# Kernel tuning notes

Measured on AMD Instinct MI355X. Metric: run time of the kernel, lower is better.

The kernel has to match this reference:

```python
import jax, jax.numpy as jnp
import numpy as np

N_NODES = 100000
N_EDGES = 1600000
IN_FEATS = 128
N_HIDDEN = 128
N_CLASSES = 40
EPS = 1e-12  # torch F.normalize eps


def _sage_conv(h, src, dst, W_self, b_self, W_neigh, b_neigh, act, norm):
    # mean aggregation over in-neighbors: dst receives from src
    agg = jax.ops.segment_sum(h[src], dst, num_segments=N_NODES)  # [N, D]
    deg = jax.ops.segment_sum(jnp.ones(dst.shape, h.dtype), dst, num_segments=N_NODES)
    h_neigh = agg / jnp.maximum(deg, 1.0)[:, None]
    out = h @ W_self + b_self + h_neigh @ W_neigh + b_neigh
    if act:
        out = jax.nn.relu(out)
    if norm:
        out = out / jnp.maximum(
            jnp.linalg.norm(out, axis=1, keepdims=True), EPS)
    return out


def setup_inputs() -> dict:
    key = jax.random.key(0)
    ks = jax.random.split(key, 16)
    def lin(k, fan_in, fan_out):
        s = 1.0 / np.sqrt(fan_in)
        return jax.random.uniform(k, (fan_in, fan_out), jnp.float32, -s, s)
    inp = {
        "features": jax.random.normal(ks[0], (N_NODES, IN_FEATS), jnp.float32),
        "src": jax.random.randint(ks[1], (N_EDGES,), 0, N_NODES, jnp.int32),
        "dst": jax.random.randint(ks[2], (N_EDGES,), 0, N_NODES, jnp.int32),
        # layer 0: in -> hidden
        "Ws0": lin(ks[3], IN_FEATS, N_HIDDEN), "bs0": jnp.zeros((N_HIDDEN,), jnp.float32),
        "Wn0": lin(ks[4], IN_FEATS, N_HIDDEN), "bn0": jnp.zeros((N_HIDDEN,), jnp.float32),
        # layer 1: hidden -> hidden
        "Ws1": lin(ks[5], N_HIDDEN, N_HIDDEN), "bs1": jnp.zeros((N_HIDDEN,), jnp.float32),
        "Wn1": lin(ks[6], N_HIDDEN, N_HIDDEN), "bn1": jnp.zeros((N_HIDDEN,), jnp.float32),
        # layer 2: hidden -> classes (no activation, no norm)
        "Ws2": lin(ks[7], N_HIDDEN, N_CLASSES), "bs2": jnp.zeros((N_CLASSES,), jnp.float32),
        "Wn2": lin(ks[8], N_HIDDEN, N_CLASSES), "bn2": jnp.zeros((N_CLASSES,), jnp.float32),
    }
    return inp


def reference(features, src, dst,
              Ws0, bs0, Wn0, bn0,
              Ws1, bs1, Wn1, bn1,
              Ws2, bs2, Wn2, bn2):
    h = _sage_conv(features, src, dst, Ws0, bs0, Wn0, bn0, act=True, norm=True)
    h = _sage_conv(h, src, dst, Ws1, bs1, Wn1, bn1, act=True, norm=True)
    out = _sage_conv(h, src, dst, Ws2, bs2, Wn2, bn2, act=False, norm=False)
    return out
```

## Files before the change

### kernel.cpp

```cpp
#include <hip/hip_runtime.h>
#include <hip/hip_bf16.h>

#define N_NODES_C 100000
#define N_EDGES_C 1600000
#define N_BUCK ((N_NODES_C + 255) / 256)
#define BCAP 4608
#define PART_NB 160
#define PART_CHUNK ((N_EDGES_C + PART_NB - 1) / PART_NB)

typedef __attribute__((ext_vector_type(8))) short          short8;
typedef __attribute__((ext_vector_type(4))) float          f32x4;
typedef __attribute__((ext_vector_type(4))) unsigned int   u32x4;
typedef __attribute__((ext_vector_type(4))) unsigned short u16x4;

__device__ inline float load1v(const void* p, size_t i, int bf) {
    return bf ? __bfloat162float(((const __hip_bfloat16*)p)[i])
              : ((const float*)p)[i];
}
__device__ inline unsigned short f2bf(float f) {
    __hip_bfloat16 h = __float2bfloat16(f);
    return *reinterpret_cast<unsigned short*>(&h);
}
__device__ inline float bf_lo(unsigned u) { return __uint_as_float(u << 16); }
__device__ inline float bf_hi(unsigned u) { return __uint_as_float(u & 0xffff0000u); }
__device__ inline void acc8(float* a, u32x4 r) {
    a[0] += bf_lo(r.x); a[1] += bf_hi(r.x);
    a[2] += bf_lo(r.y); a[3] += bf_hi(r.y);
    a[4] += bf_lo(r.z); a[5] += bf_hi(r.z);
    a[6] += bf_lo(r.w); a[7] += bf_hi(r.w);
}

__global__ void detect_init(const void* __restrict__ feats, int* __restrict__ gflag,
                            int* __restrict__ bcur) {
    const unsigned short* u = (const unsigned short*)feats;
    int bad = 0;
    for (int i = threadIdx.x; i < 2048; i += 64) {
        unsigned e = (u[i] >> 7) & 0xFF;
        if (e >= 0xC0) bad++;
    }
#pragma unroll
    for (int off = 32; off > 0; off >>= 1) bad += __shfl_down(bad, off, 64);
    if (threadIdx.x == 0) *gflag = (bad == 0) ? 1 : 0;
    for (int b = threadIdx.x; b < N_BUCK; b += 64) bcur[b] = b * BCAP;
}

__global__ __launch_bounds__(256) void partition2(
        const int* __restrict__ src, const int* __restrict__ dst,
        int* __restrict__ bcur, unsigned* __restrict__ pairs) {
    __shared__ int cnt[N_BUCK];
    __shared__ int lbase[N_BUCK];
    int tid = threadIdx.x;
    int e0 = blockIdx.x * PART_CHUNK;
    int e1 = min(e0 + PART_CHUNK, N_EDGES_C);
    for (int i = tid; i < N_BUCK; i += 256) cnt[i] = 0;
    __syncthreads();
    for (int e = e0 + tid; e < e1; e += 256)
        atomicAdd(&cnt[dst[e] >> 8], 1);
    __syncthreads();
    for (int i = tid; i < N_BUCK; i += 256) {
        int c = cnt[i];
        lbase[i] = c ? atomicAdd(&bcur[i], c) : 0;
        cnt[i] = 0;
    }
    __syncthreads();
    for (int e = e0 + tid; e < e1; e += 256) {
        int s = src[e], d = dst[e];
        int bk = d >> 8;
        int pos = lbase[bk] + atomicAdd(&cnt[bk], 1);
        pairs[pos] = ((unsigned)(d & 255) << 17) | (unsigned)s;
    }
}

__global__ void mkboff_kernel(const int* __restrict__ bcur, int* __restrict__ boff) {
    __shared__ int c[N_BUCK];
    int tid = threadIdx.x;
    for (int i = tid; i < N_BUCK; i += 64) c[i] = bcur[i] - i * BCAP;
    __syncthreads();
    if (tid == 0) {
        int run = 0;
        for (int b = 0; b < N_BUCK; ++b) { int t = c[b]; c[b] = run; run += t; }
        boff[N_BUCK] = run;
    }
    __syncthreads();
    for (int i = tid; i < N_BUCK; i += 64) boff[i] = c[i];
}

__global__ __launch_bounds__(256) void bucket_fill(
        const unsigned* __restrict__ pairs, const int* __restrict__ boff,
        int* __restrict__ csr, int* __restrict__ row_start, int* __restrict__ deg) {
    __shared__ int cnt[256], sd[256], lcur[256];
    int b = blockIdx.x, tid = threadIdx.x;
    int pbase = b * BCAP;
    int base = boff[b], count = boff[b + 1] - base;
    cnt[tid] = 0;
    __syncthreads();
    for (int i = tid; i < count; i += 256)
        atomicAdd(&cnt[pairs[pbase + i] >> 17], 1);
    __syncthreads();
    sd[tid] = cnt[tid];
    __syncthreads();
    for (int st = 1; st < 256; st <<= 1) {
        int t = (tid >= st) ? sd[tid - st] : 0;
        __syncthreads();
        sd[tid] += t;
        __syncthreads();
    }
    int excl = sd[tid] - cnt[tid];
    int node = b * 256 + tid;
    if (node < N_NODES_C) { row_start[node] = base + excl; deg[node] = cnt[tid]; }
    lcur[tid] = excl;
    __syncthreads();
    for (int i = tid; i < count; i += 256) {
        unsigned p = pairs[pbase + i];
        int pos = base + atomicAdd(&lcur[p >> 17], 1);
        csr[pos] = (int)(p & 0x1FFFFu);
    }
}

__global__ void prep_weights(const void* Ws0, const void* bs0, const void* Wn0, const void* bn0,
                             const void* Ws1, const void* bs1, const void* Wn1, const void* bn1,
                             const void* Ws2, const void* bs2, const void* Wn2, const void* bn2,
                             unsigned short* __restrict__ Wt, float* __restrict__ bcat,
                             const int* __restrict__ gflag) {
    int gb = *gflag;
    int n = blockIdx.x;
    int k = threadIdx.x;
    if (n < 128) {
        float v = (k < 128) ? load1v(Ws0, (size_t)k * 128 + n, gb)
                            : load1v(Wn0, (size_t)(k - 128) * 128 + n, gb);
        Wt[(size_t)n * 256 + k] = f2bf(v);
        if (k == 0) bcat[n] = load1v(bs0, n, gb) + load1v(bn0, n, gb);
    } else if (n < 256) {
        int c = n - 128;
        float v = (k < 128) ? load1v(Ws1, (size_t)k * 128 + c, gb)
                            : load1v(Wn1, (size_t)(k - 128) * 128 + c, gb);
        Wt[(size_t)n * 256 + k] = f2bf(v);
        if (k == 0) bcat[n] = load1v(bs1, c, gb) + load1v(bn1, c, gb);
    } else {
        int c = n - 256;
        if (k < 128) {
            float v = (c < 40) ? load1v(Ws2, (size_t)k * 40 + c, gb)
                               : load1v(Wn2, (size_t)k * 40 + (c - 40), gb);
            Wt[65536 + (size_t)c * 128 + k] = f2bf(v);
        }
        if (k == 0) bcat[n] = (c < 40) ? load1v(bs2, c, gb) + load1v(bn2, c, gb) : 0.0f;
    }
}

__global__ __launch_bounds__(256) void gather_kernel(
        const void* __restrict__ hsrc, int src_stride,
        int src_mode, int copy_self,
        const int* __restrict__ csr,
        const int* __restrict__ row_start,
        const int* __restrict__ deg,
        unsigned short* __restrict__ X,
        const int* __restrict__ gflag) {
    int wave = threadIdx.x >> 6, lane = threadIdx.x & 63;
    int g = lane >> 4, sub = lane & 15;
    int srcLane = lane & 48;
    int node = blockIdx.x * 16 + wave * 4 + g;
    bool valid = node < N_NODES_C;
    int vnode = valid ? node : (N_NODES_C - 1);
    int start = row_start[vnode];
    int d = valid ? deg[vnode] : 0;
    const int* cp = csr + start;
    float inv = (d > 0) ? 1.0f / (float)d : 0.0f;
    int bf = (src_mode == 2) ? *gflag : src_mode;

    if (bf) {
        const unsigned short* hb = (const unsigned short*)hsrc;
        float a[8] = {0, 0, 0, 0, 0, 0, 0, 0};
        for (int base = 0; base < d; base += 16) {
            int n16 = min(d - base, 16);
            int idxr = cp[base + ((sub < n16) ? sub : 0)];
            int i = 0;
            for (; i + 8 <= n16; i += 8) {
                int nb0 = __shfl(idxr, srcLane + i + 0, 64);
                int nb1 = __shfl(idxr, srcLane + i + 1, 64);
                int nb2 = __shfl(idxr, srcLane + i + 2, 64);
                int nb3 = __shfl(idxr, srcLane + i + 3, 64);
                int nb4 = __shfl(idxr, srcLane + i + 4, 64);
                int nb5 = __shfl(idxr, srcLane + i + 5, 64);
                int nb6 = __shfl(idxr, srcLane + i + 6, 64);
                int nb7 = __shfl(idxr, srcLane + i + 7, 64);
                u32x4 r0 = *(const u32x4*)(hb + (size_t)nb0 * src_stride + sub * 8);
                u32x4 r1 = *(const u32x4*)(hb + (size_t)nb1 * src_stride + sub * 8);
                u32x4 r2 = *(const u32x4*)(hb + (size_t)nb2 * src_stride + sub * 8);
                u32x4 r3 = *(const u32x4*)(hb + (size_t)nb3 * src_stride + sub * 8);
                u32x4 r4 = *(const u32x4*)(hb + (size_t)nb4 * src_stride + sub * 8);
                u32x4 r5 = *(const u32x4*)(hb + (size_t)nb5 * src_stride + sub * 8);
                u32x4 r6 = *(const u32x4*)(hb + (size_t)nb6 * src_stride + sub * 8);
                u32x4 r7 = *(const u32x4*)(hb + (size_t)nb7 * src_stride + sub * 8);
                acc8(a, r0); acc8(a, r1); acc8(a, r2); acc8(a, r3);
                acc8(a, r4); acc8(a, r5); acc8(a, r6); acc8(a, r7);
            }
            for (; i + 4 <= n16; i += 4) {
                int nb0 = __shfl(idxr, srcLane + i + 0, 64);
                int nb1 = __shfl(idxr, srcLane + i + 1, 64);
                int nb2 = __shfl(idxr, srcLane + i + 2, 64);
                int nb3 = __shfl(idxr, srcLane + i + 3, 64);
                u32x4 r0 = *(const u32x4*)(hb + (size_t)nb0 * src_stride + sub * 8);
                u32x4 r1 = *(const u32x4*)(hb + (size_t)nb1 * src_stride + sub * 8);
                u32x4 r2 = *(const u32x4*)(hb + (size_t)nb2 * src_stride + sub * 8);
                u32x4 r3 = *(const u32x4*)(hb + (size_t)nb3 * src_stride + sub * 8);
                acc8(a, r0); acc8(a, r1); acc8(a, r2); acc8(a, r3);
            }
            for (; i < n16; ++i) {
                int nb = __shfl(idxr, srcLane + i, 64);
                u32x4 r = *(const u32x4*)(hb + (size_t)nb * src_stride + sub * 8);
                acc8(a, r);
            }
        }
        if (valid) {
            u32x4 o;
            o.x = (unsigned)f2bf(a[0] * inv) | ((unsigned)f2bf(a[1] * inv) << 16);
            o.y = (unsigned)f2bf(a[2] * inv) | ((unsigned)f2bf(a[3] * inv) << 16);
            o.z = (unsigned)f2bf(a[4] * inv) | ((unsigned)f2bf(a[5] * inv) << 16);
            o.w = (unsigned)f2bf(a[6] * inv) | ((unsigned)f2bf(a[7] * inv) << 16);
            *(u32x4*)(X + (size_t)node * 256 + 128 + sub * 8) = o;
            if (copy_self) {
                u32x4 raw = *(const u32x4*)(hb + (size_t)node * src_stride + sub * 8);
                *(u32x4*)(X + (size_t)node * 256 + sub * 8) = raw;
            }
        }
    } else {
        const float* hf = (const float*)hsrc;
        float a[8] = {0, 0, 0, 0, 0, 0, 0, 0};
        for (int base = 0; base < d; base += 16) {
            int n16 = min(d - base, 16);
            int idxr = cp[base + ((sub < n16) ? sub : 0)];
            int i = 0;
            for (; i + 4 <= n16; i += 4) {
                int nb0 = __shfl(idxr, srcLane + i + 0, 64);
                int nb1 = __shfl(idxr, srcLane + i + 1, 64);
                int nb2 = __shfl(idxr, srcLane + i + 2, 64);
                int nb3 = __shfl(idxr, srcLane + i + 3, 64);
                const float* p0 = hf + (size_t)nb0 * src_stride + sub * 4;
                const float* p1 = hf + (size_t)nb1 * src_stride + sub * 4;
                const float* p2 = hf + (size_t)nb2 * src_stride + sub * 4;
                const float* p3 = hf + (size_t)nb3 * src_stride + sub * 4;
                f32x4 a0 = *(const f32x4*)p0, b0 = *(const f32x4*)(p0 + 64);
                f32x4 a1 = *(const f32x4*)p1, b1 = *(const f32x4*)(p1 + 64);
                f32x4 a2 = *(const f32x4*)p2, b2 = *(const f32x4*)(p2 + 64);
                f32x4 a3 = *(const f32x4*)p3, b3 = *(const f32x4*)(p3 + 64);
#pragma unroll
                for (int k = 0; k < 4; ++k) {
                    a[k] += a0[k] + a1[k] + a2[k] + a3[k];
                    a[4 + k] += b0[k] + b1[k] + b2[k] + b3[k];
                }
            }
            for (; i < n16; ++i) {
                int nb = __shfl(idxr, srcLane + i, 64);
                const float* p0 = hf + (size_t)nb * src_stride + sub * 4;
                f32x4 a0 = *(const f32x4*)p0, b0 = *(const f32x4*)(p0 + 64);
#pragma unroll
                for (int k = 0; k < 4; ++k) { a[k] += a0[k]; a[4 + k] += b0[k]; }
            }
        }
        if (valid) {
            u16x4 oa = { f2bf(a[0] * inv), f2bf(a[1] * inv),
                         f2bf(a[2] * inv), f2bf(a[3] * inv) };
            u16x4 ob = { f2bf(a[4] * inv), f2bf(a[5] * inv),
                         f2bf(a[6] * inv), f2bf(a[7] * inv) };
            *(u16x4*)(X + (size_t)node * 256 + 128 + sub * 4) = oa;
            *(u16x4*)(X + (size_t)node * 256 + 128 + 64 + sub * 4) = ob;
            if (copy_self) {
                const float* sp = hf + (size_t)node * src_stride + sub * 4;
                f32x4 ra = *(const f32x4*)sp;
                f32x4 rb = *(const f32x4*)(sp + 64);
                u16x4 sa = { f2bf(ra.x), f2bf(ra.y), f2bf(ra.z), f2bf(ra.w) };
                u16x4 sb = { f2bf(rb.x), f2bf(rb.y), f2bf(rb.z), f2bf(rb.w) };
                *(u16x4*)(X + (size_t)node * 256 + sub * 4) = sa;
                *(u16x4*)(X + (size_t)node * 256 + 64 + sub * 4) = sb;
            }
        }
    }
}

template <int NCT, int KT, int CHK, bool ACTNORM, bool DUAL>
__global__ __launch_bounds__(256) void mfma_gemm(
        const unsigned short* __restrict__ X, int astride,
        const u32x4* __restrict__ Wg,
        const float* __restrict__ bias,
        unsigned short* __restrict__ out, int out_stride,
        unsigned short* __restrict__ Ybuf, unsigned short* __restrict__ Zbuf,
        int n_nodes) {
    __shared__ u32x4 ldsW[NCT * 16 * CHK];
    int tid = threadIdx.x;
    for (int c = tid; c < NCT * 16 * CHK; c += 256) {
        int nrow = c / CHK, ch = c % CHK;
        ldsW[nrow * CHK + (ch ^ (nrow & 7))] = Wg[c];
    }
    __syncthreads();

    int wave = tid >> 6, lane = tid & 63;
    int quad = lane >> 4, sub = lane & 15;
    int mynode = blockIdx.x * 64 + wave * 16 + sub;
    int arow = (mynode < n_nodes) ? mynode : (n_nodes - 1);
    const unsigned short* ap = X + (size_t)arow * astride + quad * 8;

    f32x4 acc[NCT];
#pragma unroll
    for (int ct = 0; ct < NCT; ++ct) acc[ct] = (f32x4){0,0,0,0};

    short8 av = *(const short8*)ap;
#pragma unroll
    for (int kt = 0; kt < KT; ++kt) {
        short8 av_next = av;
        if (kt < KT - 1) av_next = *(const short8*)(ap + (kt + 1) * 32);
        int chunk = kt * 4 + quad;
#pragma unroll
        for (int ct = 0; ct < NCT; ++ct) {
            int ncol = ct * 16 + sub;
            union { u32x4 u; short8 s; } cv;
            cv.u = ldsW[ncol * CHK + (chunk ^ (ncol & 7))];
            acc[ct] = __builtin_amdgcn_mfma_f32_16x16x32_bf16(cv.s, av, acc[ct], 0, 0, 0);
        }
        av = av_next;
    }

    float ss = 0.0f;
#pragma unroll
    for (int ct = 0; ct < NCT; ++ct) {
        f32x4 b4 = *(const f32x4*)(bias + ct * 16 + quad * 4);
#pragma unroll
        for (int r = 0; r < 4; ++r) {
            float v = acc[ct][r] + b4[r];
            if (ACTNORM) { v = fmaxf(v, 0.0f); ss += v * v; }
            acc[ct][r] = v;
        }
    }
    float scale = 1.0f;
    if (ACTNORM) {
        ss += __shfl_xor(ss, 16, 64);
        ss += __shfl_xor(ss, 32, 64);
        scale = 1.0f / fmaxf(sqrtf(ss), 1e-12f);
    }
    if (mynode < n_nodes) {
#pragma unroll
        for (int ct = 0; ct < NCT; ++ct) {
            int c0 = ct * 16 + quad * 4;
            u16x4 o = { f2bf(acc[ct][0] * scale), f2bf(acc[ct][1] * scale),
                        f2bf(acc[ct][2] * scale), f2bf(acc[ct][3] * scale) };
            if (DUAL) {
                if (c0 < 40) *(u16x4*)(Zbuf + (size_t)mynode * 40 + c0) = o;
                else         *(u16x4*)(Ybuf + (size_t)mynode * 40 + (c0 - 40)) = o;
            } else {
                *(u16x4*)(out + (size_t)mynode * out_stride + c0) = o;
            }
        }
    }
}

__global__ void combine_kernel(const unsigned short* __restrict__ Y2,
                               const unsigned short* __restrict__ Z2,
                               const int* __restrict__ csr,
                               const int* __restrict__ row_start,
                               const int* __restrict__ deg,
                               void* __restrict__ out,
                               const int* __restrict__ gflag) {
    int node = blockIdx.x * 4 + (threadIdx.x >> 6);
    if (node >= N_NODES_C) return;
    int lane = threadIdx.x & 63;
    int g = lane >> 3, sub = lane & 7;
    int start = row_start[node], d = deg[node];
    const int* cp = csr + start;
    float a[8] = {0,0,0,0,0,0,0,0};
    int rd = (sub < 5) ? sub : 4;
    int nfull = d >> 3, rem = d & 7;
    int i = 0;
    for (; i + 2 <= nfull; i += 2) {
        int nb0 = cp[i * 8 + g];
        int nb1 = cp[i * 8 + 8 + g];
        u32x4 r0 = *(const u32x4*)(Y2 + (size_t)nb0 * 40 + rd * 8);
        u32x4 r1 = *(const u32x4*)(Y2 + (size_t)nb1 * 40 + rd * 8);
        acc8(a, r0); acc8(a, r1);
    }
    if (i < nfull) {
        int nb = cp[i * 8 + g];
        u32x4 r = *(const u32x4*)(Y2 + (size_t)nb * 40 + rd * 8);
        acc8(a, r);
    }
    if (g < rem) {
        int nb = cp[nfull * 8 + g];
        u32x4 r = *(const u32x4*)(Y2 + (size_t)nb * 40 + rd * 8);
        acc8(a, r);
    }
#pragma unroll
    for (int j = 0; j < 8; ++j) {
        a[j] += __shfl_xor(a[j], 8, 64);
        a[j] += __shfl_xor(a[j], 16, 64);
        a[j] += __shfl_xor(a[j], 32, 64);
    }
    if (g == 0 && sub < 5) {
        float inv = (d > 0) ? 1.0f / (float)d : 0.0f;
        u32x4 z = *(const u32x4*)(Z2 + (size_t)node * 40 + sub * 8);
        float v[8];
        v[0] = a[0] * inv + bf_lo(z.x); v[1] = a[1] * inv + bf_hi(z.x);
        v[2] = a[2] * inv + bf_lo(z.y); v[3] = a[3] * inv + bf_hi(z.y);
        v[4] = a[4] * inv + bf_lo(z.z); v[5] = a[5] * inv + bf_hi(z.z);
        v[6] = a[6] * inv + bf_lo(z.w); v[7] = a[7] * inv + bf_hi(z.w);
        if (*gflag) {
            u32x4 o;
            o.x = (unsigned)f2bf(v[0]) | ((unsigned)f2bf(v[1]) << 16);
            o.y = (unsigned)f2bf(v[2]) | ((unsigned)f2bf(v[3]) << 16);
            o.z = (unsigned)f2bf(v[4]) | ((unsigned)f2bf(v[5]) << 16);
            o.w = (unsigned)f2bf(v[6]) | ((unsigned)f2bf(v[7]) << 16);
            *(u32x4*)((unsigned short*)out + (size_t)node * 40 + sub * 8) = o;
        } else {
            float* op = (float*)out + (size_t)node * 40 + sub * 8;
            f32x4 o0 = { v[0], v[1], v[2], v[3] };
            f32x4 o1 = { v[4], v[5], v[6], v[7] };
            *(f32x4*)op = o0;
            *(f32x4*)(op + 4) = o1;
        }
    }
}

extern "C" void kernel_launch(void* const* d_in, const int* in_sizes, int n_in,
                              void* d_out, int out_size, void* d_ws, size_t ws_size,
                              hipStream_t stream) {
    const void* feats = d_in[0];
    const int*  src   = (const int*)d_in[1];
    const int*  dst   = (const int*)d_in[2];

    char* ws = (char*)d_ws;
    unsigned short* X0   = (unsigned short*)ws;
    unsigned short* X1   = (unsigned short*)(ws + 51200000);
    unsigned short* Wt   = (unsigned short*)(ws + 102400000);
    float*          bcat = (float*)(ws + 102912000);
    unsigned short* Y2   = (unsigned short*)(ws + 102916096);
    unsigned short* Z2   = (unsigned short*)(ws + 115716096);
    unsigned*       pairs= (unsigned*)(ws + 102916096);
    int*  csr       = (int*)(ws + 128516096);
    int*  row_start = (int*)(ws + 134916096);
    int*  deg       = (int*)(ws + 135316096);
    int*  boff      = (int*)(ws + 135718144);
    int*  bcur      = (int*)(ws + 135720192);
    int*  gflag     = (int*)(ws + 135722240);

    detect_init<<<1, 64, 0, stream>>>(feats, gflag, bcur);

    partition2<<<PART_NB, 256, 0, stream>>>(src, dst, bcur, pairs);
    mkboff_kernel<<<1, 64, 0, stream>>>(bcur, boff);
    bucket_fill<<<N_BUCK, 256, 0, stream>>>(pairs, boff, csr, row_start, deg);

    prep_weights<<<336, 256, 0, stream>>>(
        d_in[3], d_in[4], d_in[5], d_in[6],
        d_in[7], d_in[8], d_in[9], d_in[10],
        d_in[11], d_in[12], d_in[13], d_in[14], Wt, bcat, gflag);

    const int gblk = (N_NODES_C + 15) / 16;
    const int cblk = (N_NODES_C + 3) / 4;
    const int mblk = (N_NODES_C + 63) / 64;

    gather_kernel<<<gblk, 256, 0, stream>>>(feats, 128, 2, 1, csr, row_start, deg, X0, gflag);
    mfma_gemm<8, 8, 32, true, false><<<mblk, 256, 0, stream>>>(
        X0, 256, (const u32x4*)Wt, bcat, X1, 256, nullptr, nullptr, N_NODES_C);

    gather_kernel<<<gblk, 256, 0, stream>>>(X1, 256, 1, 0, csr, row_start, deg, X1, gflag);
    mfma_gemm<8, 8, 32, true, false><<<mblk, 256, 0, stream>>>(
        X1, 256, (const u32x4*)(Wt + 128 * 256), bcat + 128, X0, 256, nullptr, nullptr, N_NODES_C);

    mfma_gemm<5, 4, 16, false, true><<<mblk, 256, 0, stream>>>(
        X0, 256, (const u32x4*)(Wt + 65536), bcat + 256, nullptr, 0, Y2, Z2, N_NODES_C);

    combine_kernel<<<cblk, 256, 0, stream>>>(Y2, Z2, csr, row_start, deg, d_out, gflag);
}
```

Measured before the change: 463.4 us.

## Fuse neighbor gather with MFMA GEMM per layer via LDS staging

Replaces the separate gather kernel and MFMA GEMM for layers 0 and 1 with a single fused kernel. Each block gathers and mean-aggregates 64 nodes into a swizzled LDS tile, then runs the dense bf16 MFMA, ReLU and L2 normalization on it. Hidden activations are stored compactly at 128 columns instead of as 256-column concatenated X buffers. This removes the global write and reread of the intermediate X matrix, at the cost of larger LDS use per block, weights reloaded in two halves, and lower occupancy during the gather.

```diff
diff --git a/kernel.cpp b/kernel.cpp
--- a/kernel.cpp
+++ b/kernel.cpp
@@ -7,6 +7,8 @@
 #define BCAP 4608
 #define PART_NB 160
 #define PART_CHUNK ((N_EDGES_C + PART_NB - 1) / PART_NB)
+
+#define FB_NODES 64
 
 typedef __attribute__((ext_vector_type(8))) short          short8;
 typedef __attribute__((ext_vector_type(4))) float          f32x4;
@@ -28,6 +30,9 @@
     a[2] += bf_lo(r.y); a[3] += bf_hi(r.y);
     a[4] += bf_lo(r.z); a[5] += bf_hi(r.z);
     a[6] += bf_lo(r.w); a[7] += bf_hi(r.w);
+}
+__device__ inline int xaddr(int l, int byteCol) {
+    return l * 512 + ((((byteCol >> 4) ^ (l & 7)) << 4)) + (byteCol & 15);
 }
 
 __global__ void detect_init(const void* __restrict__ feats, int* __restrict__ gflag,
@@ -147,132 +152,188 @@
     }
 }
 
-__global__ __launch_bounds__(256) void gather_kernel(
-        const void* __restrict__ hsrc, int src_stride,
-        int src_mode, int copy_self,
-        const int* __restrict__ csr,
-        const int* __restrict__ row_start,
+__global__ __launch_bounds__(256) void fused_layer(
+        const void* __restrict__ hsrc, int src_stride, int src_mode,
+        const int* __restrict__ csr, const int* __restrict__ row_start,
         const int* __restrict__ deg,
-        unsigned short* __restrict__ X,
-        const int* __restrict__ gflag) {
-    int wave = threadIdx.x >> 6, lane = threadIdx.x & 63;
+        const u32x4* __restrict__ Wg,
+        const float* __restrict__ bias,
+        unsigned short* __restrict__ hout,
+        int n_nodes, const int* __restrict__ gflag) {
+    __shared__ u32x4 xt4[FB_NODES * 32];
+    __shared__ u32x4 ldsW[128 * 16];
+    char* xt = (char*)xt4;
+
+    int tid = threadIdx.x;
+    int wave = tid >> 6, lane = tid & 63;
     int g = lane >> 4, sub = lane & 15;
     int srcLane = lane & 48;
-    int node = blockIdx.x * 16 + wave * 4 + g;
-    bool valid = node < N_NODES_C;
-    int vnode = valid ? node : (N_NODES_C - 1);
-    int start = row_start[vnode];
-    int d = valid ? deg[vnode] : 0;
-    const int* cp = csr + start;
-    float inv = (d > 0) ? 1.0f / (float)d : 0.0f;
     int bf = (src_mode == 2) ? *gflag : src_mode;
-
-    if (bf) {
-        const unsigned short* hb = (const unsigned short*)hsrc;
-        float a[8] = {0, 0, 0, 0, 0, 0, 0, 0};
-        for (int base = 0; base < d; base += 16) {
-            int n16 = min(d - base, 16);
-            int idxr = cp[base + ((sub < n16) ? sub : 0)];
-            int i = 0;
-            for (; i + 8 <= n16; i += 8) {
-                int nb0 = __shfl(idxr, srcLane + i + 0, 64);
-                int nb1 = __shfl(idxr, srcLane + i + 1, 64);
-                int nb2 = __shfl(idxr, srcLane + i + 2, 64);
-                int nb3 = __shfl(idxr, srcLane + i + 3, 64);
-                int nb4 = __shfl(idxr, srcLane + i + 4, 64);
-                int nb5 = __shfl(idxr, srcLane + i + 5, 64);
-                int nb6 = __shfl(idxr, srcLane + i + 6, 64);
-                int nb7 = __shfl(idxr, srcLane + i + 7, 64);
-                u32x4 r0 = *(const u32x4*)(hb + (size_t)nb0 * src_stride + sub * 8);
-                u32x4 r1 = *(const u32x4*)(hb + (size_t)nb1 * src_stride + sub * 8);
-                u32x4 r2 = *(const u32x4*)(hb + (size_t)nb2 * src_stride + sub * 8);
-                u32x4 r3 = *(const u32x4*)(hb + (size_t)nb3 * src_stride + sub * 8);
-                u32x4 r4 = *(const u32x4*)(hb + (size_t)nb4 * src_stride + sub * 8);
-                u32x4 r5 = *(const u32x4*)(hb + (size_t)nb5 * src_stride + sub * 8);
-                u32x4 r6 = *(const u32x4*)(hb + (size_t)nb6 * src_stride + sub * 8);
-                u32x4 r7 = *(const u32x4*)(hb + (size_t)nb7 * src_stride + sub * 8);
-                acc8(a, r0); acc8(a, r1); acc8(a, r2); acc8(a, r3);
-                acc8(a, r4); acc8(a, r5); acc8(a, r6); acc8(a, r7);
+    int nb0 = blockIdx.x * FB_NODES;
+
+    for (int t = 0; t < 4; ++t) {
+        int l = (wave * 4 + g) * 4 + t;
+        int node = nb0 + l;
+        bool valid = node < n_nodes;
+        int vnode = valid ? node : (n_nodes - 1);
+        int start = row_start[vnode];
+        int d = valid ? deg[vnode] : 0;
+        const int* cp = csr + start;
+        float inv = (d > 0) ? 1.0f / (float)d : 0.0f;
+
+        if (bf) {
+            const unsigned short* hb = (const unsigned short*)hsrc;
+            float a[8] = {0, 0, 0, 0, 0, 0, 0, 0};
+            for (int base = 0; base < d; base += 16) {
+                int n16 = min(d - base, 16);
+                int idxr = cp[base + ((sub < n16) ? sub : 0)];
+                int i = 0;
+                for (; i + 8 <= n16; i += 8) {
+                    int nb_0 = __shfl(idxr, srcLane + i + 0, 64);
+                    int nb_1 = __shfl(idxr, srcLane + i + 1, 64);
+                    int nb_2 = __shfl(idxr, srcLane + i + 2, 64);
+                    int nb_3 = __shfl(idxr, srcLane + i + 3, 64);
+                    int nb_4 = __shfl(idxr, srcLane + i + 4, 64);
+                    int nb_5 = __shfl(idxr, srcLane + i + 5, 64);
+                    int nb_6 = __shfl(idxr, srcLane + i + 6, 64);
+                    int nb_7 = __shfl(idxr, srcLane + i + 7, 64);
+                    u32x4 r0 = *(const u32x4*)(hb + (size_t)nb_0 * src_stride + sub * 8);
+                    u32x4 r1 = *(const u32x4*)(hb + (size_t)nb_1 * src_stride + sub * 8);
+                    u32x4 r2 = *(const u32x4*)(hb + (size_t)nb_2 * src_stride + sub * 8);
+                    u32x4 r3 = *(const u32x4*)(hb + (size_t)nb_3 * src_stride + sub * 8);
+                    u32x4 r4 = *(const u32x4*)(hb + (size_t)nb_4 * src_stride + sub * 8);
+                    u32x4 r5 = *(const u32x4*)(hb + (size_t)nb_5 * src_stride + sub * 8);
+                    u32x4 r6 = *(const u32x4*)(hb + (size_t)nb_6 * src_stride + sub * 8);
+                    u32x4 r7 = *(const u32x4*)(hb + (size_t)nb_7 * src_stride + sub * 8);
+                    acc8(a, r0); acc8(a, r1); acc8(a, r2); acc8(a, r3);
+                    acc8(a, r4); acc8(a, r5); acc8(a, r6); acc8(a, r7);
+                }
+                for (; i + 4 <= n16; i += 4) {
+                    int nb_0 = __shfl(idxr, srcLane + i + 0, 64);
+                    int nb_1 = __shfl(idxr, srcLane + i + 1, 64);
+                    int nb_2 = __shfl(idxr, srcLane + i + 2, 64);
+                    int nb_3 = __shfl(idxr, srcLane + i + 3, 64);
+                    u32x4 r0 = *(const u32x4*)(hb + (size_t)nb_0 * src_stride + sub * 8);
+                    u32x4 r1 = *(const u32x4*)(hb + (size_t)nb_1 * src_stride + sub * 8);
+                    u32x4 r2 = *(const u32x4*)(hb + (size_t)nb_2 * src_stride + sub * 8);
+                    u32x4 r3 = *(const u32x4*)(hb + (size_t)nb_3 * src_stride + sub * 8);
+                    acc8(a, r0); acc8(a, r1); acc8(a, r2); acc8(a, r3);
+                }
+                for (; i < n16; ++i) {
+                    int nb_ = __shfl(idxr, srcLane + i, 64);
+                    u32x4 r = *(const u32x4*)(hb + (size_t)nb_ * src_stride + sub * 8);
+                    acc8(a, r);
+                }
             }
-            for (; i + 4 <= n16; i += 4) {
-                int nb0 = __shfl(idxr, srcLane + i + 0, 64);
-                int nb1 = __shfl(idxr, srcLane + i + 1, 64);
-                int nb2 = __shfl(idxr, srcLane + i + 2, 64);
-                int nb3 = __shfl(idxr, srcLane + i + 3, 64);
-                u32x4 r0 = *(const u32x4*)(hb + (size_t)nb0 * src_stride + sub * 8);
-                u32x4 r1 = *(const u32x4*)(hb + (size_t)nb1 * src_stride + sub * 8);
-                u32x4 r2 = *(const u32x4*)(hb + (size_t)nb2 * src_stride + sub * 8);
-                u32x4 r3 = *(const u32x4*)(hb + (size_t)nb3 * src_stride + sub * 8);
-                acc8(a, r0); acc8(a, r1); acc8(a, r2); acc8(a, r3);
-            }
-            for (; i < n16; ++i) {
-                int nb = __shfl(idxr, srcLane + i, 64);
-                u32x4 r = *(const u32x4*)(hb + (size_t)nb * src_stride + sub * 8);
-                acc8(a, r);
-            }
-        }
-        if (valid) {
             u32x4 o;
             o.x = (unsigned)f2bf(a[0] * inv) | ((unsigned)f2bf(a[1] * inv) << 16);
             o.y = (unsigned)f2bf(a[2] * inv) | ((unsigned)f2bf(a[3] * inv) << 16);
             o.z = (unsigned)f2bf(a[4] * inv) | ((unsigned)f2bf(a[5] * inv) << 16);
             o.w = (unsigned)f2bf(a[6] * inv) | ((unsigned)f2bf(a[7] * inv) << 16);
-            *(u32x4*)(X + (size_t)node * 256 + 128 + sub * 8) = o;
-            if (copy_self) {
-                u32x4 raw = *(const u32x4*)(hb + (size_t)node * src_stride + sub * 8);
-                *(u32x4*)(X + (size_t)node * 256 + sub * 8) = raw;
-            }
-        }
-    } else {
-        const float* hf = (const float*)hsrc;
-        float a[8] = {0, 0, 0, 0, 0, 0, 0, 0};
-        for (int base = 0; base < d; base += 16) {
-            int n16 = min(d - base, 16);
-            int idxr = cp[base + ((sub < n16) ? sub : 0)];
-            int i = 0;
-            for (; i + 4 <= n16; i += 4) {
-                int nb0 = __shfl(idxr, srcLane + i + 0, 64);
-                int nb1 = __shfl(idxr, srcLane + i + 1, 64);
-                int nb2 = __shfl(idxr, srcLane + i + 2, 64);
-                int nb3 = __shfl(idxr, srcLane + i + 3, 64);
-                const float* p0 = hf + (size_t)nb0 * src_stride + sub * 4;
-                const float* p1 = hf + (size_t)nb1 * src_stride + sub * 4;
-                const float* p2 = hf + (size_t)nb2 * src_stride + sub * 4;
-                const float* p3 = hf + (size_t)nb3 * src_stride + sub * 4;
-                f32x4 a0 = *(const f32x4*)p0, b0 = *(const f32x4*)(p0 + 64);
-                f32x4 a1 = *(const f32x4*)p1, b1 = *(const f32x4*)(p1 + 64);
-                f32x4 a2 = *(const f32x4*)p2, b2 = *(const f32x4*)(p2 + 64);
-                f32x4 a3 = *(const f32x4*)p3, b3 = *(const f32x4*)(p3 + 64);
-#pragma unroll
-                for (int k = 0; k < 4; ++k) {
-                    a[k] += a0[k] + a1[k] + a2[k] + a3[k];
-                    a[4 + k] += b0[k] + b1[k] + b2[k] + b3[k];
+            *(u32x4*)(xt + xaddr(l, 256 + sub * 16)) = o;
+            u32x4 raw = *(const u32x4*)(hb + (size_t)vnode * src_stride + sub * 8);
+            *(u32x4*)(xt + xaddr(l, sub * 16)) = raw;
+        } else {
+            const float* hf = (const float*)hsrc;
+            float a[8] = {0, 0, 0, 0, 0, 0, 0, 0};
+            for (int base = 0; base < d; base += 16) {
+                int n16 = min(d - base, 16);
+                int idxr = cp[base + ((sub < n16) ? sub : 0)];
+                int i = 0;
+                for (; i + 4 <= n16; i += 4) {
+                    int nb_0 = __shfl(idxr, srcLane + i + 0, 64);
+                    int nb_1 = __shfl(idxr, srcLane + i + 1, 64);
+                    int nb_2 = __shfl(idxr, srcLane + i + 2, 64);
+                    int nb_3 = __shfl(idxr, srcLane + i + 3, 64);
+                    const float* p0 = hf + (size_t)nb_0 * src_stride + sub * 4;
+                    const float* p1 = hf + (size_t)nb_1 * src_stride + sub * 4;
+                    const float* p2 = hf + (size_t)nb_2 * src_stride + sub * 4;
+                    const float* p3 = hf + (size_t)nb_3 * src_stride + sub * 4;
+                    f32x4 a0 = *(const f32x4*)p0, b0 = *(const f32x4*)(p0 + 64);
+                    f32x4 a1 = *(const f32x4*)p1, b1 = *(const f32x4*)(p1 + 64);
+                    f32x4 a2 = *(const f32x4*)p2, b2 = *(const f32x4*)(p2 + 64);
+                    f32x4 a3 = *(const f32x4*)p3, b3 = *(const f32x4*)(p3 + 64);
+#pragma unroll
+                    for (int k = 0; k < 4; ++k) {
+                        a[k] += a0[k] + a1[k] + a2[k] + a3[k];
+                        a[4 + k] += b0[k] + b1[k] + b2[k] + b3[k];
+                    }
+                }
+                for (; i < n16; ++i) {
+                    int nb_ = __shfl(idxr, srcLane + i, 64);
+                    const float* p0 = hf + (size_t)nb_ * src_stride + sub * 4;
+                    f32x4 a0 = *(const f32x4*)p0, b0 = *(const f32x4*)(p0 + 64);
+#pragma unroll
+                    for (int k = 0; k < 4; ++k) { a[k] += a0[k]; a[4 + k] += b0[k]; }
                 }
             }
-            for (; i < n16; ++i) {
-                int nb = __shfl(idxr, srcLane + i, 64);
-                const float* p0 = hf + (size_t)nb * src_stride + sub * 4;
-                f32x4 a0 = *(const f32x4*)p0, b0 = *(const f32x4*)(p0 + 64);
-#pragma unroll
-                for (int k = 0; k < 4; ++k) { a[k] += a0[k]; a[4 + k] += b0[k]; }
-            }
-        }
-        if (valid) {
             u16x4 oa = { f2bf(a[0] * inv), f2bf(a[1] * inv),
                          f2bf(a[2] * inv), f2bf(a[3] * inv) };
             u16x4 ob = { f2bf(a[4] * inv), f2bf(a[5] * inv),
                          f2bf(a[6] * inv), f2bf(a[7] * inv) };
-            *(u16x4*)(X + (size_t)node * 256 + 128 + sub * 4) = oa;
-            *(u16x4*)(X + (size_t)node * 256 + 128 + 64 + sub * 4) = ob;
-            if (copy_self) {
-                const float* sp = hf + (size_t)node * src_stride + sub * 4;
-                f32x4 ra = *(const f32x4*)sp;
-                f32x4 rb = *(const f32x4*)(sp + 64);
-                u16x4 sa = { f2bf(ra.x), f2bf(ra.y), f2bf(ra.z), f2bf(ra.w) };
-                u16x4 sb = { f2bf(rb.x), f2bf(rb.y), f2bf(rb.z), f2bf(rb.w) };
-                *(u16x4*)(X + (size_t)node * 256 + sub * 4) = sa;
-                *(u16x4*)(X + (size_t)node * 256 + 64 + sub * 4) = sb;
+            *(u16x4*)(xt + xaddr(l, 256 + sub * 8)) = oa;
+            *(u16x4*)(xt + xaddr(l, 384 + sub * 8)) = ob;
+            const float* sp = hf + (size_t)vnode * src_stride + sub * 4;
+            f32x4 ra = *(const f32x4*)sp;
+            f32x4 rb = *(const f32x4*)(sp + 64);
+            u16x4 sa = { f2bf(ra.x), f2bf(ra.y), f2bf(ra.z), f2bf(ra.w) };
+            u16x4 sb = { f2bf(rb.x), f2bf(rb.y), f2bf(rb.z), f2bf(rb.w) };
+            *(u16x4*)(xt + xaddr(l, sub * 8)) = sa;
+            *(u16x4*)(xt + xaddr(l, 128 + sub * 8)) = sb;
+        }
+    }
+
+    int quad = g;
+    int lrow = wave * 16 + sub;
+    int mynode = nb0 + lrow;
+
+    f32x4 acc[8];
+#pragma unroll
+    for (int ct = 0; ct < 8; ++ct) acc[ct] = (f32x4){0, 0, 0, 0};
+
+    for (int half = 0; half < 2; ++half) {
+        __syncthreads();
+        for (int c = tid; c < 128 * 16; c += 256) {
+            int nrow = c >> 4, ch = c & 15;
+            ldsW[(nrow << 4) + (ch ^ (nrow & 7))] = Wg[nrow * 32 + half * 16 + ch];
+        }
+        __syncthreads();
+#pragma unroll
+        for (int kt4 = 0; kt4 < 4; ++kt4) {
+            int kt = half * 4 + kt4;
+            short8 av = *(const short8*)(xt + xaddr(lrow, quad * 16 + kt * 64));
+            int chunk = kt4 * 4 + quad;
+#pragma unroll
+            for (int ct = 0; ct < 8; ++ct) {
+                int ncol = ct * 16 + sub;
+                union { u32x4 u; short8 s; } cv;
+                cv.u = ldsW[(ncol << 4) + (chunk ^ (ncol & 7))];
+                acc[ct] = __builtin_amdgcn_mfma_f32_16x16x32_bf16(cv.s, av, acc[ct], 0, 0, 0);
             }
+        }
+    }
+
+    float ss = 0.0f;
+#pragma unroll
+    for (int ct = 0; ct < 8; ++ct) {
+        f32x4 b4 = *(const f32x4*)(bias + ct * 16 + quad * 4);
+#pragma unroll
+        for (int r = 0; r < 4; ++r) {
+            float v = acc[ct][r] + b4[r];
+            v = fmaxf(v, 0.0f); ss += v * v;
+            acc[ct][r] = v;
+        }
+    }
+    ss += __shfl_xor(ss, 16, 64);
+    ss += __shfl_xor(ss, 32, 64);
+    float scale = 1.0f / fmaxf(sqrtf(ss), 1e-12f);
+    if (mynode < n_nodes) {
+#pragma unroll
+        for (int ct = 0; ct < 8; ++ct) {
+            int c0 = ct * 16 + quad * 4;
+            u16x4 o = { f2bf(acc[ct][0] * scale), f2bf(acc[ct][1] * scale),
+                        f2bf(acc[ct][2] * scale), f2bf(acc[ct][3] * scale) };
+            *(u16x4*)(hout + (size_t)mynode * 128 + c0) = o;
         }
     }
 }
@@ -425,8 +486,8 @@
     const int*  dst   = (const int*)d_in[2];
 
     char* ws = (char*)d_ws;
-    unsigned short* X0   = (unsigned short*)ws;
-    unsigned short* X1   = (unsigned short*)(ws + 51200000);
+    unsigned short* H1   = (unsigned short*)ws;
+    unsigned short* H2   = (unsigned short*)(ws + 25600000);
     unsigned short* Wt   = (unsigned short*)(ws + 102400000);
     float*          bcat = (float*)(ws + 102912000);
     unsigned short* Y2   = (unsigned short*)(ws + 102916096);
@@ -450,20 +511,20 @@
         d_in[7], d_in[8], d_in[9], d_in[10],
         d_in[11], d_in[12], d_in[13], d_in[14], Wt, bcat, gflag);
 
-    const int gblk = (N_NODES_C + 15) / 16;
+    const int fblk = (N_NODES_C + FB_NODES - 1) / FB_NODES;
     const int cblk = (N_NODES_C + 3) / 4;
     const int mblk = (N_NODES_C + 63) / 64;
 
-    gather_kernel<<<gblk, 256, 0, stream>>>(feats, 128, 2, 1, csr, row_start, deg, X0, gflag);
-    mfma_gemm<8, 8, 32, true, false><<<mblk, 256, 0, stream>>>(
-        X0, 256, (const u32x4*)Wt, bcat, X1, 256, nullptr, nullptr, N_NODES_C);
-
-    gather_kernel<<<gblk, 256, 0, stream>>>(X1, 256, 1, 0, csr, row_start, deg, X1, gflag);
-    mfma_gemm<8, 8, 32, true, false><<<mblk, 256, 0, stream>>>(
-        X1, 256, (const u32x4*)(Wt + 128 * 256), bcat + 128, X0, 256, nullptr, nullptr, N_NODES_C);
+    fused_layer<<<fblk, 256, 0, stream>>>(
+        feats, 128, 2, csr, row_start, deg,
+        (const u32x4*)Wt, bcat, H1, N_NODES_C, gflag);
+
+    fused_layer<<<fblk, 256, 0, stream>>>(
+        H1, 128, 1, csr, row_start, deg,
+        (const u32x4*)(Wt + 128 * 256), bcat + 128, H2, N_NODES_C, gflag);
 
     mfma_gemm<5, 4, 16, false, true><<<mblk, 256, 0, stream>>>(
-        X0, 256, (const u32x4*)(Wt + 65536), bcat + 256, nullptr, 0, Y2, Z2, N_NODES_C);
+        H2, 128, (const u32x4*)(Wt + 65536), bcat + 256, nullptr, 0, Y2, Z2, N_NODES_C);
 
     combine_kernel<<<cblk, 256, 0, stream>>>(Y2, Z2, csr, row_start, deg, d_out, gflag);
 }
```

After: 491.9 us. +6.1%, slower.

## Split self and mean operands into separate buffers and skip self-copy

Applied to the files above, without the earlier changes.

The gather kernel now writes only the neighbor mean into a compact 128-wide buffer instead of the right half of a 256-wide concatenated row. The bf16 self-feature copy is dropped. A new GEMM kernel reads the self rows directly from the source (original features if bf16, otherwise a converted copy) and the mean rows from the separate buffer. This is meant to cut redundant copy traffic and halve the stride of the gathered rows, which improves cache density for the neighbor gathers in layer 2. The cost is two separate A-operand streams in the GEMM.

```diff
diff --git a/kernel.cpp b/kernel.cpp
--- a/kernel.cpp
+++ b/kernel.cpp
@@ -153,7 +153,8 @@
         const int* __restrict__ csr,
         const int* __restrict__ row_start,
         const int* __restrict__ deg,
-        unsigned short* __restrict__ X,
+        unsigned short* __restrict__ Xmean,
+        unsigned short* __restrict__ Sout,
         const int* __restrict__ gflag) {
     int wave = threadIdx.x >> 6, lane = threadIdx.x & 63;
     int g = lane >> 4, sub = lane & 15;
@@ -217,11 +218,7 @@
             o.y = (unsigned)f2bf(a[2] * inv) | ((unsigned)f2bf(a[3] * inv) << 16);
             o.z = (unsigned)f2bf(a[4] * inv) | ((unsigned)f2bf(a[5] * inv) << 16);
             o.w = (unsigned)f2bf(a[6] * inv) | ((unsigned)f2bf(a[7] * inv) << 16);
-            *(u32x4*)(X + (size_t)node * 256 + 128 + sub * 8) = o;
-            if (copy_self) {
-                u32x4 raw = *(const u32x4*)(hb + (size_t)node * src_stride + sub * 8);
-                *(u32x4*)(X + (size_t)node * 256 + sub * 8) = raw;
-            }
+            *(u32x4*)(Xmean + (size_t)node * 128 + sub * 8) = o;
         }
     } else {
         const float* hf = (const float*)hsrc;
@@ -262,17 +259,92 @@
                          f2bf(a[2] * inv), f2bf(a[3] * inv) };
             u16x4 ob = { f2bf(a[4] * inv), f2bf(a[5] * inv),
                          f2bf(a[6] * inv), f2bf(a[7] * inv) };
-            *(u16x4*)(X + (size_t)node * 256 + 128 + sub * 4) = oa;
-            *(u16x4*)(X + (size_t)node * 256 + 128 + 64 + sub * 4) = ob;
+            *(u16x4*)(Xmean + (size_t)node * 128 + sub * 4) = oa;
+            *(u16x4*)(Xmean + (size_t)node * 128 + 64 + sub * 4) = ob;
             if (copy_self) {
                 const float* sp = hf + (size_t)node * src_stride + sub * 4;
                 f32x4 ra = *(const f32x4*)sp;
                 f32x4 rb = *(const f32x4*)(sp + 64);
                 u16x4 sa = { f2bf(ra.x), f2bf(ra.y), f2bf(ra.z), f2bf(ra.w) };
                 u16x4 sb = { f2bf(rb.x), f2bf(rb.y), f2bf(rb.z), f2bf(rb.w) };
-                *(u16x4*)(X + (size_t)node * 256 + sub * 4) = sa;
-                *(u16x4*)(X + (size_t)node * 256 + 64 + sub * 4) = sb;
-            }
+                *(u16x4*)(Sout + (size_t)node * 128 + sub * 4) = sa;
+                *(u16x4*)(Sout + (size_t)node * 128 + 64 + sub * 4) = sb;
+            }
+        }
+    }
+}
+
+__global__ __launch_bounds__(256) void mfma_gemm_split(
+        const unsigned short* __restrict__ AselfA,
+        const unsigned short* __restrict__ AselfB,
+        const unsigned short* __restrict__ Amean,
+        const u32x4* __restrict__ Wg,
+        const float* __restrict__ bias,
+        unsigned short* __restrict__ hout,
+        int n_nodes, const int* __restrict__ gflag, int use_flag) {
+    __shared__ u32x4 ldsW[128 * 32];
+    int tid = threadIdx.x;
+    for (int c = tid; c < 128 * 32; c += 256) {
+        int nrow = c >> 5, ch = c & 31;
+        ldsW[(nrow << 5) + (ch ^ (nrow & 7))] = Wg[c];
+    }
+    __syncthreads();
+
+    const unsigned short* Aself = AselfA;
+    if (use_flag && *gflag == 0) Aself = AselfB;
+
+    int wave = tid >> 6, lane = tid & 63;
+    int quad = lane >> 4, sub = lane & 15;
+    int mynode = blockIdx.x * 64 + wave * 16 + sub;
+    int arow = (mynode < n_nodes) ? mynode : (n_nodes - 1);
+    const unsigned short* apS = Aself + (size_t)arow * 128 + quad * 8;
+    const unsigned short* apM = Amean + (size_t)arow * 128 + quad * 8;
+
+    f32x4 acc[8];
+#pragma unroll
+    for (int ct = 0; ct < 8; ++ct) acc[ct] = (f32x4){0, 0, 0, 0};
+
+    short8 av = *(const short8*)apS;
+#pragma unroll
+    for (int kt = 0; kt < 8; ++kt) {
+        short8 av_next = av;
+        if (kt < 7) {
+            int kn = kt + 1;
+            av_next = (kn < 4) ? *(const short8*)(apS + kn * 32)
+                               : *(const short8*)(apM + (kn - 4) * 32);
+        }
+        int chunk = kt * 4 + quad;
+#pragma unroll
+        for (int ct = 0; ct < 8; ++ct) {
+            int ncol = ct * 16 + sub;
+            union { u32x4 u; short8 s; } cv;
+            cv.u = ldsW[(ncol << 5) + (chunk ^ (ncol & 7))];
+            acc[ct] = __builtin_amdgcn_mfma_f32_16x16x32_bf16(cv.s, av, acc[ct], 0, 0, 0);
+        }
+        av = av_next;
+    }
+
+    float ss = 0.0f;
+#pragma unroll
+    for (int ct = 0; ct < 8; ++ct) {
+        f32x4 b4 = *(const f32x4*)(bias + ct * 16 + quad * 4);
+#pragma unroll
+        for (int r = 0; r < 4; ++r) {
+            float v = acc[ct][r] + b4[r];
+            v = fmaxf(v, 0.0f); ss += v * v;
+            acc[ct][r] = v;
+        }
+    }
+    ss += __shfl_xor(ss, 16, 64);
+    ss += __shfl_xor(ss, 32, 64);
+    float scale = 1.0f / fmaxf(sqrtf(ss), 1e-12f);
+    if (mynode < n_nodes) {
+#pragma unroll
+        for (int ct = 0; ct < 8; ++ct) {
+            int c0 = ct * 16 + quad * 4;
+            u16x4 o = { f2bf(acc[ct][0] * scale), f2bf(acc[ct][1] * scale),
+                        f2bf(acc[ct][2] * scale), f2bf(acc[ct][3] * scale) };
+            *(u16x4*)(hout + (size_t)mynode * 128 + c0) = o;
         }
     }
 }
@@ -425,8 +497,10 @@
     const int*  dst   = (const int*)d_in[2];
 
     char* ws = (char*)d_ws;
-    unsigned short* X0   = (unsigned short*)ws;
-    unsigned short* X1   = (unsigned short*)(ws + 51200000);
+    unsigned short* MEAN = (unsigned short*)ws;
+    unsigned short* H1   = (unsigned short*)(ws + 25600000);
+    unsigned short* H2   = (unsigned short*)(ws + 51200000);
+    unsigned short* S0   = (unsigned short*)(ws + 76800000);
     unsigned short* Wt   = (unsigned short*)(ws + 102400000);
     float*          bcat = (float*)(ws + 102912000);
     unsigned short* Y2   = (unsigned short*)(ws + 102916096);
@@ -454,16 +528,20 @@
     const int cblk = (N_NODES_C + 3) / 4;
     const int mblk = (N_NODES_C + 63) / 64;
 
-    gather_kernel<<<gblk, 256, 0, stream>>>(feats, 128, 2, 1, csr, row_start, deg, X0, gflag);
-    mfma_gemm<8, 8, 32, true, false><<<mblk, 256, 0, stream>>>(
-        X0, 256, (const u32x4*)Wt, bcat, X1, 256, nullptr, nullptr, N_NODES_C);
-
-    gather_kernel<<<gblk, 256, 0, stream>>>(X1, 256, 1, 0, csr, row_start, deg, X1, gflag);
-    mfma_gemm<8, 8, 32, true, false><<<mblk, 256, 0, stream>>>(
-        X1, 256, (const u32x4*)(Wt + 128 * 256), bcat + 128, X0, 256, nullptr, nullptr, N_NODES_C);
+    gather_kernel<<<gblk, 256, 0, stream>>>(feats, 128, 2, 1, csr, row_start, deg,
+                                            MEAN, S0, gflag);
+    mfma_gemm_split<<<mblk, 256, 0, stream>>>(
+        (const unsigned short*)feats, S0, MEAN,
+        (const u32x4*)Wt, bcat, H1, N_NODES_C, gflag, 1);
+
+    gather_kernel<<<gblk, 256, 0, stream>>>(H1, 128, 1, 0, csr, row_start, deg,
+                                            MEAN, nullptr, gflag);
+    mfma_gemm_split<<<mblk, 256, 0, stream>>>(
+        H1, H1, MEAN,
+        (const u32x4*)(Wt + 128 * 256), bcat + 128, H2, N_NODES_C, gflag, 0);
 
     mfma_gemm<5, 4, 16, false, true><<<mblk, 256, 0, stream>>>(
-        X0, 256, (const u32x4*)(Wt + 65536), bcat + 256, nullptr, 0, Y2, Z2, N_NODES_C);
+        H2, 128, (const u32x4*)(Wt + 65536), bcat + 256, nullptr, 0, Y2, Z2, N_NODES_C);
 
     combine_kernel<<<cblk, 256, 0, stream>>>(Y2, Z2, csr, row_start, deg, d_out, gflag);
 }
```

Result: no change. 469.9 us (+1.4%).

## Remap combine to one 8-lane group per node and fold bucket offsets into fill

Applied to the files above, without the earlier changes.

The final combine kernel now gives each node an 8-lane group instead of a whole wave. Each group loads up to 8 neighbor indices at once, broadcasts them with shuffles, and issues 8 independent row loads, so the cross-group shuffle reduction is gone. To keep these loads aligned, the Y2/Z2 intermediate buffers get a padded 64-element row stride, which wastes bandwidth on the 24 padding columns. The single-thread mkboff prefix kernel is removed. Each bucket_fill block now computes its own base offset by reducing bcur over all earlier buckets, which saves one serial launch at the cost of redundant per-block reads.

```diff
diff --git a/kernel.cpp b/kernel.cpp
--- a/kernel.cpp
+++ b/kernel.cpp
@@ -71,27 +71,24 @@
     }
 }
 
-__global__ void mkboff_kernel(const int* __restrict__ bcur, int* __restrict__ boff) {
-    __shared__ int c[N_BUCK];
-    int tid = threadIdx.x;
-    for (int i = tid; i < N_BUCK; i += 64) c[i] = bcur[i] - i * BCAP;
-    __syncthreads();
-    if (tid == 0) {
-        int run = 0;
-        for (int b = 0; b < N_BUCK; ++b) { int t = c[b]; c[b] = run; run += t; }
-        boff[N_BUCK] = run;
-    }
-    __syncthreads();
-    for (int i = tid; i < N_BUCK; i += 64) boff[i] = c[i];
-}
-
 __global__ __launch_bounds__(256) void bucket_fill(
-        const unsigned* __restrict__ pairs, const int* __restrict__ boff,
+        const unsigned* __restrict__ pairs, const int* __restrict__ bcur,
         int* __restrict__ csr, int* __restrict__ row_start, int* __restrict__ deg) {
     __shared__ int cnt[256], sd[256], lcur[256];
     int b = blockIdx.x, tid = threadIdx.x;
     int pbase = b * BCAP;
-    int base = boff[b], count = boff[b + 1] - base;
+
+    int psum = 0;
+    for (int i = tid; i < b; i += 256) psum += bcur[i] - i * BCAP;
+    sd[tid] = psum;
+    __syncthreads();
+    for (int st = 128; st > 0; st >>= 1) {
+        if (tid < st) sd[tid] += sd[tid + st];
+        __syncthreads();
+    }
+    int base = sd[0];
+    int count = bcur[b] - b * BCAP;
+
     cnt[tid] = 0;
     __syncthreads();
     for (int i = tid; i < count; i += 256)
@@ -343,8 +340,8 @@
             u16x4 o = { f2bf(acc[ct][0] * scale), f2bf(acc[ct][1] * scale),
                         f2bf(acc[ct][2] * scale), f2bf(acc[ct][3] * scale) };
             if (DUAL) {
-                if (c0 < 40) *(u16x4*)(Zbuf + (size_t)mynode * 40 + c0) = o;
-                else         *(u16x4*)(Ybuf + (size_t)mynode * 40 + (c0 - 40)) = o;
+                if (c0 < 40) *(u16x4*)(Zbuf + (size_t)mynode * 64 + c0) = o;
+                else         *(u16x4*)(Ybuf + (size_t)mynode * 64 + (c0 - 40)) = o;
             } else {
                 *(u16x4*)(out + (size_t)mynode * out_stride + c0) = o;
             }
@@ -352,67 +349,79 @@
     }
 }
 
-__global__ void combine_kernel(const unsigned short* __restrict__ Y2,
-                               const unsigned short* __restrict__ Z2,
-                               const int* __restrict__ csr,
-                               const int* __restrict__ row_start,
-                               const int* __restrict__ deg,
-                               void* __restrict__ out,
-                               const int* __restrict__ gflag) {
-    int node = blockIdx.x * 4 + (threadIdx.x >> 6);
-    if (node >= N_NODES_C) return;
-    int lane = threadIdx.x & 63;
-    int g = lane >> 3, sub = lane & 7;
-    int start = row_start[node], d = deg[node];
+__global__ __launch_bounds__(256) void combine_kernel(
+        const unsigned short* __restrict__ Y2,
+        const unsigned short* __restrict__ Z2,
+        const int* __restrict__ csr,
+        const int* __restrict__ row_start,
+        const int* __restrict__ deg,
+        void* __restrict__ out,
+        const int* __restrict__ gflag) {
+    int wave = threadIdx.x >> 6, lane = threadIdx.x & 63;
+    int grp = lane >> 3, sub = lane & 7;
+    int grpLane = lane & 56;
+    int node = blockIdx.x * 32 + wave * 8 + grp;
+    bool valid = node < N_NODES_C;
+    int vnode = valid ? node : (N_NODES_C - 1);
+    int start = row_start[vnode];
+    int d = valid ? deg[vnode] : 0;
     const int* cp = csr + start;
-    float a[8] = {0,0,0,0,0,0,0,0};
-    int rd = (sub < 5) ? sub : 4;
-    int nfull = d >> 3, rem = d & 7;
-    int i = 0;
-    for (; i + 2 <= nfull; i += 2) {
-        int nb0 = cp[i * 8 + g];
-        int nb1 = cp[i * 8 + 8 + g];
-        u32x4 r0 = *(const u32x4*)(Y2 + (size_t)nb0 * 40 + rd * 8);
-        u32x4 r1 = *(const u32x4*)(Y2 + (size_t)nb1 * 40 + rd * 8);
-        acc8(a, r0); acc8(a, r1);
-    }
-    if (i < nfull) {
-        int nb = cp[i * 8 + g];
-        u32x4 r = *(const u32x4*)(Y2 + (size_t)nb * 40 + rd * 8);
-        acc8(a, r);
-    }
-    if (g < rem) {
-        int nb = cp[nfull * 8 + g];
-        u32x4 r = *(const u32x4*)(Y2 + (size_t)nb * 40 + rd * 8);
-        acc8(a, r);
-    }
-#pragma unroll
-    for (int j = 0; j < 8; ++j) {
-        a[j] += __shfl_xor(a[j], 8, 64);
-        a[j] += __shfl_xor(a[j], 16, 64);
-        a[j] += __shfl_xor(a[j], 32, 64);
-    }
-    if (g == 0 && sub < 5) {
+
+    float a[8] = {0, 0, 0, 0, 0, 0, 0, 0};
+    for (int base = 0; base < d; base += 8) {
+        int n8 = min(d - base, 8);
+        int idxr = cp[base + ((sub < n8) ? sub : 0)];
+        if (n8 == 8) {
+            int nb0 = __shfl(idxr, grpLane + 0, 64);
+            int nb1 = __shfl(idxr, grpLane + 1, 64);
+            int nb2 = __shfl(idxr, grpLane + 2, 64);
+            int nb3 = __shfl(idxr, grpLane + 3, 64);
+            int nb4 = __shfl(idxr, grpLane + 4, 64);
+            int nb5 = __shfl(idxr, grpLane + 5, 64);
+            int nb6 = __shfl(idxr, grpLane + 6, 64);
+            int nb7 = __shfl(idxr, grpLane + 7, 64);
+            u32x4 r0 = *(const u32x4*)(Y2 + (size_t)nb0 * 64 + sub * 8);
+            u32x4 r1 = *(const u32x4*)(Y2 + (size_t)nb1 * 64 + sub * 8);
+            u32x4 r2 = *(const u32x4*)(Y2 + (size_t)nb2 * 64 + sub * 8);
+            u32x4 r3 = *(const u32x4*)(Y2 + (size_t)nb3 * 64 + sub * 8);
+            u32x4 r4 = *(const u32x4*)(Y2 + (size_t)nb4 * 64 + sub * 8);
+            u32x4 r5 = *(const u32x4*)(Y2 + (size_t)nb5 * 64 + sub * 8);
+            u32x4 r6 = *(const u32x4*)(Y2 + (size_t)nb6 * 64 + sub * 8);
+            u32x4 r7 = *(const u32x4*)(Y2 + (size_t)nb7 * 64 + sub * 8);
+            acc8(a, r0); acc8(a, r1); acc8(a, r2); acc8(a, r3);
+            acc8(a, r4); acc8(a, r5); acc8(a, r6); acc8(a, r7);
+        } else {
+            for (int j = 0; j < n8; ++j) {
+                int nb = __shfl(idxr, grpLane + j, 64);
+                u32x4 r = *(const u32x4*)(Y2 + (size_t)nb * 64 + sub * 8);
+                acc8(a, r);
+            }
+        }
+    }
+
+    if (valid) {
         float inv = (d > 0) ? 1.0f / (float)d : 0.0f;
-        u32x4 z = *(const u32x4*)(Z2 + (size_t)node * 40 + sub * 8);
+        u32x4 z = *(const u32x4*)(Z2 + (size_t)node * 64 + sub * 8);
         float v[8];
         v[0] = a[0] * inv + bf_lo(z.x); v[1] = a[1] * inv + bf_hi(z.x);
         v[2] = a[2] * inv + bf_lo(z.y); v[3] = a[3] * inv + bf_hi(z.y);
         v[4] = a[4] * inv + bf_lo(z.z); v[5] = a[5] * inv + bf_hi(z.z);
         v[6] = a[6] * inv + bf_lo(z.w); v[7] = a[7] * inv + bf_hi(z.w);
-        if (*gflag) {
-            u32x4 o;
-            o.x = (unsigned)f2bf(v[0]) | ((unsigned)f2bf(v[1]) << 16);
-            o.y = (unsigned)f2bf(v[2]) | ((unsigned)f2bf(v[3]) << 16);
-            o.z = (unsigned)f2bf(v[4]) | ((unsigned)f2bf(v[5]) << 16);
-            o.w = (unsigned)f2bf(v[6]) | ((unsigned)f2bf(v[7]) << 16);
-            *(u32x4*)((unsigned short*)out + (size_t)node * 40 + sub * 8) = o;
-        } else {
-            float* op = (float*)out + (size_t)node * 40 + sub * 8;
-            f32x4 o0 = { v[0], v[1], v[2], v[3] };
-            f32x4 o1 = { v[4], v[5], v[6], v[7] };
-            *(f32x4*)op = o0;
-            *(f32x4*)(op + 4) = o1;
+        if (sub < 5) {
+            if (*gflag) {
+                u32x4 o;
+                o.x = (unsigned)f2bf(v[0]) | ((unsigned)f2bf(v[1]) << 16);
+                o.y = (unsigned)f2bf(v[2]) | ((unsigned)f2bf(v[3]) << 16);
+                o.z = (unsigned)f2bf(v[4]) | ((unsigned)f2bf(v[5]) << 16);
+                o.w = (unsigned)f2bf(v[6]) | ((unsigned)f2bf(v[7]) << 16);
+                *(u32x4*)((unsigned short*)out + (size_t)node * 40 + sub * 8) = o;
+            } else {
+                float* op = (float*)out + (size_t)node * 40 + sub * 8;
+                f32x4 o0 = { v[0], v[1], v[2], v[3] };
+                f32x4 o1 = { v[4], v[5], v[6], v[7] };
+                *(f32x4*)op = o0;
+                *(f32x4*)(op + 4) = o1;
+            }
         }
     }
 }
@@ -435,15 +444,13 @@
     int*  csr       = (int*)(ws + 128516096);
     int*  row_start = (int*)(ws + 134916096);
     int*  deg       = (int*)(ws + 135316096);
-    int*  boff      = (int*)(ws + 135718144);
     int*  bcur      = (int*)(ws + 135720192);
     int*  gflag     = (int*)(ws + 135722240);
 
     detect_init<<<1, 64, 0, stream>>>(feats, gflag, bcur);
 
     partition2<<<PART_NB, 256, 0, stream>>>(src, dst, bcur, pairs);
-    mkboff_kernel<<<1, 64, 0, stream>>>(bcur, boff);
-    bucket_fill<<<N_BUCK, 256, 0, stream>>>(pairs, boff, csr, row_start, deg);
+    bucket_fill<<<N_BUCK, 256, 0, stream>>>(pairs, bcur, csr, row_start, deg);
 
     prep_weights<<<336, 256, 0, stream>>>(
         d_in[3], d_in[4], d_in[5], d_in[6],
@@ -451,7 +458,7 @@
         d_in[11], d_in[12], d_in[13], d_in[14], Wt, bcat, gflag);
 
     const int gblk = (N_NODES_C + 15) / 16;
-    const int cblk = (N_NODES_C + 3) / 4;
+    const int cblk = (N_NODES_C + 31) / 32;
     const int mblk = (N_NODES_C + 63) / 64;
 
     gather_kernel<<<gblk, 256, 0, stream>>>(feats, 128, 2, 1, csr, row_start, deg, X0, gflag);
```

After: 460.8 us. No clear change (-0.6%).
